# Kernel tuning notes

Hardware: AMD Instinct MI355X
Metric: run time of the kernel (lower is better)

Reference implementation:

```python
import jax, jax.numpy as jnp
import numpy as np
from functools import partial

IN_CH, OUT_CH, HID = 16, 20, 256
B, T = 64, 4096
LEAKY_SLOPE = 0.01  # torch LeakyReLU default


def _lstm_layer(x_seq, Wih, Whh, bih, bhh):
    """Single-layer LSTM over a full sequence.

    x_seq: (T, B, Din). Weights use PyTorch layout: W (4H, Din/H), gate order i,f,g,o.
    Returns hidden states (T, B, H).
    """
    H = Whh.shape[1]
    Tlen, Bsz = x_seq.shape[0], x_seq.shape[1]
    # Precompute input contributions for all timesteps in one GEMM.
    xw = jnp.einsum('tbd,gd->tbg', x_seq, Wih) + (bih + bhh)  # (T, B, 4H)

    def step(carry, xw_t):
        h, c = carry
        gates = xw_t + h @ Whh.T  # (B, 4H)
        i, f, g, o = jnp.split(gates, 4, axis=-1)
        i = jax.nn.sigmoid(i)
        f = jax.nn.sigmoid(f)
        g = jnp.tanh(g)
        o = jax.nn.sigmoid(o)
        c = f * c + i * g
        h = o * jnp.tanh(c)
        return (h, c), h

    h0 = jnp.zeros((Bsz, H), dtype=x_seq.dtype)
    c0 = jnp.zeros((Bsz, H), dtype=x_seq.dtype)
    _, hs = jax.lax.scan(step, (h0, c0), xw)
    return hs  # (T, B, H)


def setup_inputs() -> dict:
    key = jax.random.key(0)
    ks = jax.random.split(key, 12)
    s = 1.0 / np.sqrt(HID)  # torch nn.LSTM init scale
    return {
        'x': jax.random.normal(ks[0], (B, IN_CH, T), dtype=jnp.float32),
        'Wih0': jax.random.normal(ks[1], (4 * HID, IN_CH), dtype=jnp.float32) * s,
        'Whh0': jax.random.normal(ks[2], (4 * HID, HID), dtype=jnp.float32) * s,
        'bih0': jax.random.normal(ks[3], (4 * HID,), dtype=jnp.float32) * s,
        'bhh0': jax.random.normal(ks[4], (4 * HID,), dtype=jnp.float32) * s,
        'Wih1': jax.random.normal(ks[5], (4 * HID, HID), dtype=jnp.float32) * s,
        'Whh1': jax.random.normal(ks[6], (4 * HID, HID), dtype=jnp.float32) * s,
        'bih1': jax.random.normal(ks[7], (4 * HID,), dtype=jnp.float32) * s,
        'bhh1': jax.random.normal(ks[8], (4 * HID,), dtype=jnp.float32) * s,
        'Whead': jax.random.normal(ks[9], (OUT_CH, HID), dtype=jnp.float32) * s,
        'bhead': jax.random.normal(ks[10], (OUT_CH,), dtype=jnp.float32) * s,
    }


def reference(x, Wih0, Whh0, bih0, bhh0, Wih1, Whh1, bih1, bhh1, Whead, bhead):
    # x: (B, C_in, T) -> time-major (T, B, C_in)
    xs = jnp.transpose(x, (2, 0, 1))
    h1 = _lstm_layer(xs, Wih0, Whh0, bih0, bhh0)   # (T, B, H)
    h2 = _lstm_layer(h1, Wih1, Whh1, bih1, bhh1)   # (T, B, H)
    # Head: LeakyReLU then Linear, applied per timestep (vectorized).
    a = jnp.where(h2 >= 0, h2, LEAKY_SLOPE * h2)
    y = jnp.einsum('tbh,oh->tbo', a, Whead) + bhead  # (T, B, OUT)
    return jnp.transpose(y, (1, 2, 0))  # (B, C_out, T)
```

## Files before the change

### kernel.cpp

```cpp
#include <hip/hip_runtime.h>
#include <hip/hip_fp16.h>
#include <stdint.h>


#define T_SEQ 4096
#define NB    64
#define HID   256
#define G4    1024
#define INCH  16
#define OC    20

typedef _Float16 h2v   __attribute__((ext_vector_type(2)));
typedef _Float16 f16x8 __attribute__((ext_vector_type(8)));
typedef float    f32x4 __attribute__((ext_vector_type(4)));

__device__ __forceinline__ float fdot2(uint32_t a, uint32_t b, float c) {
  return __builtin_amdgcn_fdot2(__builtin_bit_cast(h2v, a),
                                __builtin_bit_cast(h2v, b), c, false);
}
__device__ __forceinline__ float sigf(float x) {
  x = fminf(fmaxf(x, -30.f), 30.f);
  return 1.f / (1.f + __expf(-x));
}
__device__ __forceinline__ float tanhf_fast(float x) {
  x = fminf(fmaxf(x, -15.f), 15.f);
  float e = __expf(-2.f * x);
  return (1.f - e) / (1.f + e);
}

#define PIN(x) asm volatile("" : "+v"(x))

struct SmemR {
  __half w[256 * 264];
  uint32_t hbuf[2][144];
  float bsum[1024];
  union {
    uint32_t xb[512 * 8];
    struct {
      __half abuf[2][320];
      __half whd[20 * 264];
      float  bh[20];
    } h1;
  } u;
};
struct SmemG {
  __half a[128 * 40];
  __half b[64 * 40];
};
union Smem { SmemR r; SmemG g; };

struct Params {
  const float* x;
  const __half *wh0, *wh1, *wi0, *wi1, *whd;
  const float  *bs0, *bs1, *bhd;
  float *h0s, *c0s, *h1s, *c1s;
  __half* h1w; const __half* h1r;
  float* xww;  const float* xwr;
  float* y;
  int L, Tc, nch;
};

template <int LAYER>
__device__ void role_rec(SmemR& S, int ch, const Params& P, int b) {
  if (ch < 0 || ch >= P.nch) return;
  const int tid   = threadIdx.x;
  const int slice = tid & 3;
  const int rg    = tid >> 2;
  const int Tc    = P.Tc;
  const __half* whh = (LAYER == 0) ? P.wh0 : P.wh1;

  for (int i = tid; i < 8192; i += 512) {
    int R = i >> 5, oct = i & 31;
    *(uint4*)&S.w[R * 264 + oct * 8] =
        *((const uint4*)(whh + (768 + R) * 256) + oct);
  }
  {
    const float* bs = (LAYER == 0) ? P.bs0 : P.bs1;
    for (int i = tid; i < 1024; i += 512) S.bsum[i] = bs[i];
  }
  const int t0 = ch * Tc;
  if (LAYER == 0) {
    for (int i = tid; i < Tc * 8; i += 512) {
      int dp = i / Tc, tt = i - dp * Tc;
      float v0 = P.x[(b * INCH + 2 * dp) * T_SEQ + t0 + tt];
      float v1 = P.x[(b * INCH + 2 * dp + 1) * T_SEQ + t0 + tt];
      uint32_t pv = (uint32_t)__half_as_ushort(__float2half(v0)) |
                    ((uint32_t)__half_as_ushort(__float2half(v1)) << 16);
      S.u.xb[tt * 8 + dp] = pv;
    }
  } else {
    for (int i = tid; i < OC * 256; i += 512) {
      int o = i >> 8, k = i & 255;
      S.u.h1.whd[o * 264 + k] = P.whd[i];
    }
    if (tid < OC) S.u.h1.bh[tid] = P.bhd[tid];
  }

  uint32_t wr[6][32];
#pragma unroll
  for (int j = 0; j < 6; j++) {
    const uint4* p = (const uint4*)(whh + (rg + 128 * j) * 256 + slice * 64);
#pragma unroll
    for (int q = 0; q < 8; q++) {
      uint4 v = p[q];
      wr[j][4 * q] = v.x; wr[j][4 * q + 1] = v.y;
      wr[j][4 * q + 2] = v.z; wr[j][4 * q + 3] = v.w;
    }
  }
#pragma unroll
  for (int j = 0; j < 6; j++)
#pragma unroll
    for (int q = 0; q < 32; q++) PIN(wr[j][q]);

  uint32_t wx[8][2];
  if (LAYER == 0) {
#pragma unroll
    for (int j = 0; j < 8; j++) {
      const uint32_t* p = (const uint32_t*)(P.wi0 + (rg + 128 * j) * INCH + slice * 4);
      wx[j][0] = p[0]; wx[j][1] = p[1];
    }
#pragma unroll
    for (int j = 0; j < 8; j++) { PIN(wx[j][0]); PIN(wx[j][1]); }
  }

  float* hs = (LAYER == 0) ? P.h0s : P.h1s;
  float* cs = (LAYER == 0) ? P.c0s : P.c1s;
  float hA = 0.f, hB = 0.f, cA = 0.f, cB = 0.f;
  if (slice == 0) {
    if (ch != 0) {
      hA = hs[b * 256 + rg];       cA = cs[b * 256 + rg];
      hB = hs[b * 256 + rg + 128]; cB = cs[b * 256 + rg + 128];
    }
    __half* hb = (__half*)S.hbuf[0];
    hb[(rg >> 6) * 72 + (rg & 63)] = __float2half(hA);
    hb[(2 + (rg >> 6)) * 72 + (rg & 63)] = __float2half(hB);
  }
  float xwpre[8];
  if (LAYER == 1 && slice == 0) {
#pragma unroll
    for (int j = 0; j < 8; j++)
      xwpre[j] = P.xwr[(0 * NB + b) * G4 + rg + 128 * j];
  }
  __syncthreads();

  for (int tt = 0; tt < Tc; ++tt) {
    const __half* hb = (const __half*)S.hbuf[tt & 1];
    float acc[8];
#pragma unroll
    for (int j = 0; j < 8; j++) acc[j] = 0.f;

#pragma unroll
    for (int hf = 0; hf < 2; ++hf) {
      uint32_t hh[16];
      const uint4* hp = (const uint4*)(hb + slice * 72 + hf * 32);
#pragma unroll
      for (int q = 0; q < 4; q++) {
        uint4 v = hp[q];
        hh[4 * q] = v.x; hh[4 * q + 1] = v.y; hh[4 * q + 2] = v.z; hh[4 * q + 3] = v.w;
      }
#pragma unroll
      for (int j = 0; j < 6; j++) {
        float a = acc[j];
#pragma unroll
        for (int q = 0; q < 16; q++) a = fdot2(wr[j][hf * 16 + q], hh[q], a);
        acc[j] = a;
      }
#pragma unroll
      for (int j = 6; j < 8; j++) {
        const uint4* wp =
            (const uint4*)&S.w[((j - 6) * 128 + rg) * 264 + slice * 64 + hf * 32];
        float a = acc[j];
#pragma unroll
        for (int q = 0; q < 4; q++) {
          uint4 v = wp[q];
          a = fdot2(v.x, hh[4 * q], a);
          a = fdot2(v.y, hh[4 * q + 1], a);
          a = fdot2(v.z, hh[4 * q + 2], a);
          a = fdot2(v.w, hh[4 * q + 3], a);
        }
        acc[j] = a;
      }
    }
    if (LAYER == 0) {
      uint32_t xv0 = S.u.xb[tt * 8 + 2 * slice];
      uint32_t xv1 = S.u.xb[tt * 8 + 2 * slice + 1];
#pragma unroll
      for (int j = 0; j < 8; j++) {
        acc[j] = fdot2(wx[j][0], xv0, acc[j]);
        acc[j] = fdot2(wx[j][1], xv1, acc[j]);
      }
    }
#pragma unroll
    for (int j = 0; j < 8; j++) {
      acc[j] += __shfl_xor(acc[j], 1);
      acc[j] += __shfl_xor(acc[j], 2);
    }

    if (slice == 0) {
      float g[8];
#pragma unroll
      for (int j = 0; j < 8; j++) g[j] = acc[j] + S.bsum[rg + 128 * j];
      if (LAYER == 1) {
#pragma unroll
        for (int j = 0; j < 8; j++) g[j] += xwpre[j];
        if (tt + 1 < Tc) {
#pragma unroll
          for (int j = 0; j < 8; j++)
            xwpre[j] = P.xwr[((tt + 1) * NB + b) * G4 + rg + 128 * j];
        }
      }
      float iA = sigf(g[0]), iB = sigf(g[1]);
      float fA = sigf(g[2]), fB = sigf(g[3]);
      float gA = tanhf_fast(g[4]), gB = tanhf_fast(g[5]);
      float oA = sigf(g[6]), oB = sigf(g[7]);
      cA = fA * cA + iA * gA;
      cB = fB * cB + iB * gB;
      hA = oA * tanhf_fast(cA);
      hB = oB * tanhf_fast(cB);
      __half hA16 = __float2half(hA), hB16 = __float2half(hB);
      __half* hw = (__half*)S.hbuf[(tt + 1) & 1];
      hw[(rg >> 6) * 72 + (rg & 63)] = hA16;
      hw[(2 + (rg >> 6)) * 72 + (rg & 63)] = hB16;
      if (LAYER == 0) {
        __half* dst = P.h1w + (size_t)(tt * NB + b) * 256;
        dst[rg] = hA16;
        dst[rg + 128] = hB16;
      } else {
        float aA = hA > 0.f ? hA : 0.01f * hA;
        float aB = hB > 0.f ? hB : 0.01f * hB;
        __half* ab = S.u.h1.abuf[tt & 1];
        ab[(rg >> 5) * 40 + (rg & 31)] = __float2half(aA);
        ab[(4 + (rg >> 5)) * 40 + (rg & 31)] = __float2half(aB);
      }
    }
    __syncthreads();

    if (LAYER == 1 && tid < OC * 8) {
      int o = tid >> 3, ks = tid & 7;
      const uint4* wp = (const uint4*)&S.u.h1.whd[o * 264 + ks * 32];
      const uint4* ap = (const uint4*)&S.u.h1.abuf[tt & 1][ks * 40];
      float a = 0.f;
#pragma unroll
      for (int q = 0; q < 4; q++) {
        uint4 w4 = wp[q];
        uint4 a4 = ap[q];
        a = fdot2(w4.x, a4.x, a);
        a = fdot2(w4.y, a4.y, a);
        a = fdot2(w4.z, a4.z, a);
        a = fdot2(w4.w, a4.w, a);
      }
      a += __shfl_xor(a, 1);
      a += __shfl_xor(a, 2);
      a += __shfl_xor(a, 4);
      if (ks == 0) P.y[(b * OC + o) * T_SEQ + t0 + tt] = a + S.u.h1.bh[o];
    }
  }
  if (slice == 0) {
    hs[b * 256 + rg] = hA;        cs[b * 256 + rg] = cA;
    hs[b * 256 + rg + 128] = hB;  cs[b * 256 + rg + 128] = cB;
  }
}

__device__ void role_gemm(SmemG& S, int chG, const Params& P) {
  if (chG < 0 || chG >= P.nch) return;
  const int bid = blockIdx.x - 128;
  const int nt = bid & 15, mt = bid >> 4;
  const int tb0 = mt * 128, g0 = nt * 64;
  const int tid = threadIdx.x, lane = tid & 63, w = tid >> 6;
  const int wm = w & 3, wn = w >> 2;

  f32x4 cacc[2][2] = {};
  for (int kk = 0; kk < 256; kk += 32) {
    __syncthreads();
    {
      int row = tid >> 2, q = tid & 3;
      const uint4* src = (const uint4*)(P.h1r + (tb0 + row) * 256 + kk + q * 8);
      *(uint4*)&S.a[row * 40 + q * 8] = *src;
    }
    if (tid < 256) {
      int row = tid >> 2, q = tid & 3;
      const uint4* src = (const uint4*)(P.wi1 + (g0 + row) * 256 + kk + q * 8);
      *(uint4*)&S.b[row * 40 + q * 8] = *src;
    }
    __syncthreads();
    f16x8 af[2], bf[2];
#pragma unroll
    for (int mi = 0; mi < 2; mi++)
      af[mi] = *(const f16x8*)&S.a[(wm * 32 + mi * 16 + (lane & 15)) * 40 + (lane >> 4) * 8];
#pragma unroll
    for (int ni = 0; ni < 2; ni++)
      bf[ni] = *(const f16x8*)&S.b[(wn * 32 + ni * 16 + (lane & 15)) * 40 + (lane >> 4) * 8];
#pragma unroll
    for (int mi = 0; mi < 2; mi++)
#pragma unroll
      for (int ni = 0; ni < 2; ni++)
        cacc[mi][ni] = __builtin_amdgcn_mfma_f32_16x16x32_f16(af[mi], bf[ni], cacc[mi][ni], 0, 0, 0);
  }
#pragma unroll
  for (int mi = 0; mi < 2; mi++)
#pragma unroll
    for (int ni = 0; ni < 2; ni++) {
      int m = wm * 32 + mi * 16 + (lane >> 4) * 4;
      int n = g0 + wn * 32 + ni * 16 + (lane & 15);
#pragma unroll
      for (int r = 0; r < 4; r++)
        P.xww[(size_t)(tb0 + m + r) * G4 + n] = cacc[mi][ni][r];
    }
}

__global__ __launch_bounds__(512)
__attribute__((amdgpu_waves_per_eu(2, 2)))
void fused_kernel(Params P) {
  __shared__ Smem S;
  int bid = blockIdx.x;
  if (bid < 64)        role_rec<0>(S.r, P.L, P, bid);
  else if (bid < 128)  role_rec<1>(S.r, P.L - 2, P, bid - 64);
  else                 role_gemm(S.g, P.L - 1, P);
}

__global__ void prep_kernel(const float* Wih0, const float* Whh0,
                            const float* bih0, const float* bhh0,
                            const float* Wih1, const float* Whh1,
                            const float* bih1, const float* bhh1,
                            const float* Whead, const float* bhead,
                            __half* wh0, __half* wh1, __half* wi1, __half* wi0,
                            __half* whd, float* bs0, float* bs1, float* bhd) {
  int i = blockIdx.x * blockDim.x + threadIdx.x;
  if (i < G4 * HID) {
    wh0[i] = __float2half(Whh0[i]);
    wh1[i] = __float2half(Whh1[i]);
    wi1[i] = __float2half(Wih1[i]);
  }
  if (i < G4 * INCH) wi0[i] = __float2half(Wih0[i]);
  if (i < OC * HID)  whd[i] = __float2half(Whead[i]);
  if (i < G4) { bs0[i] = bih0[i] + bhh0[i]; bs1[i] = bih1[i] + bhh1[i]; }
  if (i < OC) bhd[i] = bhead[i];
}

extern "C" void kernel_launch(void* const* d_in, const int* in_sizes, int n_in,
                              void* d_out, int out_size, void* d_ws, size_t ws_size,
                              hipStream_t stream) {
  const float* x     = (const float*)d_in[0];
  const float* Wih0  = (const float*)d_in[1];
  const float* Whh0  = (const float*)d_in[2];
  const float* bih0  = (const float*)d_in[3];
  const float* bhh0  = (const float*)d_in[4];
  const float* Wih1  = (const float*)d_in[5];
  const float* Whh1  = (const float*)d_in[6];
  const float* bih1  = (const float*)d_in[7];
  const float* bhh1  = (const float*)d_in[8];
  const float* Whead = (const float*)d_in[9];
  const float* bhead = (const float*)d_in[10];
  float* y = (float*)d_out;

  char* ws = (char*)d_ws;
  size_t cur = 0;
  auto alloc = [&](size_t sz) -> char* {
    char* p = ws + cur;
    cur = (cur + sz + 255) & ~(size_t)255;
    return p;
  };
  __half* wh0 = (__half*)alloc(G4 * HID * 2);
  __half* wh1 = (__half*)alloc(G4 * HID * 2);
  __half* wi1 = (__half*)alloc(G4 * HID * 2);
  __half* wi0 = (__half*)alloc(G4 * INCH * 2);
  __half* whd = (__half*)alloc(OC * HID * 2);
  float* bs0 = (float*)alloc(G4 * 4);
  float* bs1 = (float*)alloc(G4 * 4);
  float* bhd = (float*)alloc(OC * 4);
  float* h0s = (float*)alloc(NB * HID * 4);
  float* c0s = (float*)alloc(NB * HID * 4);
  float* h1s = (float*)alloc(NB * HID * 4);
  float* c1s = (float*)alloc(NB * HID * 4);
  size_t fixed = cur;

  int Tc = 512;
  while (Tc > 64) {
    size_t need = fixed + 2 * ((size_t)Tc * NB * HID * 2 + 512) +
                  2 * ((size_t)Tc * NB * G4 * 4 + 512);
    if (need <= ws_size) break;
    Tc >>= 1;
  }
  __half* h1buf[2];
  float* xwbuf[2];
  h1buf[0] = (__half*)alloc((size_t)Tc * NB * HID * 2);
  h1buf[1] = (__half*)alloc((size_t)Tc * NB * HID * 2);
  xwbuf[0] = (float*)alloc((size_t)Tc * NB * G4 * 4);
  xwbuf[1] = (float*)alloc((size_t)Tc * NB * G4 * 4);

  const int nch = T_SEQ / Tc;

  prep_kernel<<<(G4 * HID + 255) / 256, 256, 0, stream>>>(
      Wih0, Whh0, bih0, bhh0, Wih1, Whh1, bih1, bhh1, Whead, bhead,
      wh0, wh1, wi1, wi0, whd, bs0, bs1, bhd);

  const int ngemm = Tc * 8;
  for (int L = 0; L < nch + 2; ++L) {
    Params P;
    P.x = x;
    P.wh0 = wh0; P.wh1 = wh1; P.wi0 = wi0; P.wi1 = wi1; P.whd = whd;
    P.bs0 = bs0; P.bs1 = bs1; P.bhd = bhd;
    P.h0s = h0s; P.c0s = c0s; P.h1s = h1s; P.c1s = c1s;
    P.h1w = h1buf[L & 1];
    P.h1r = h1buf[(L + 1) & 1];
    P.xww = xwbuf[(L + 1) & 1];
    P.xwr = xwbuf[L & 1];
    P.y = y;
    P.L = L; P.Tc = Tc; P.nch = nch;
    fused_kernel<<<128 + ngemm, 512, 0, stream>>>(P);
  }
}
```

Measured before the change: 10.87 ms.

## Store xw in fp16, distribute bias/xw adds across slices, swizzle LDS weights

The precomputed input-projection buffer for layer 1 is stored in fp16 instead of fp32, halving its global traffic and workspace, which may also allow a larger time chunk. Bias and xw terms are now added per slice before the shuffle reduction, so all four lanes share the loads instead of slice 0 doing eight serial global loads. The shared-memory copy of the last two gate blocks is re-laid out so each lane reads contiguous 16-byte words, and the hidden-state and activation buffer strides are padded to change bank mapping. The cost is reduced precision of the xw term.

```diff
diff --git a/kernel.cpp b/kernel.cpp
--- a/kernel.cpp
+++ b/kernel.cpp
@@ -31,13 +31,12 @@
 #define PIN(x) asm volatile("" : "+v"(x))
 
 struct SmemR {
-  __half w[256 * 264];
-  uint32_t hbuf[2][144];
-  float bsum[1024];
+  uint32_t w[8 * 16 * 256];
+  __half hbuf[2][4 * 80];
   union {
     uint32_t xb[512 * 8];
     struct {
-      __half abuf[2][320];
+      __half abuf[2][8 * 48];
       __half whd[20 * 264];
       float  bh[20];
     } h1;
@@ -55,7 +54,7 @@
   const float  *bs0, *bs1, *bhd;
   float *h0s, *c0s, *h1s, *c1s;
   __half* h1w; const __half* h1r;
-  float* xww;  const float* xwr;
+  __half* xww; const __half* xwr;
   float* y;
   int L, Tc, nch;
 };
@@ -66,18 +65,22 @@
   const int tid   = threadIdx.x;
   const int slice = tid & 3;
   const int rg    = tid >> 2;
+  const int wv    = tid >> 6;
+  const int ln    = tid & 63;
   const int Tc    = P.Tc;
   const __half* whh = (LAYER == 0) ? P.wh0 : P.wh1;
 
-  for (int i = tid; i < 8192; i += 512) {
-    int R = i >> 5, oct = i & 31;
-    *(uint4*)&S.w[R * 264 + oct * 8] =
-        *((const uint4*)(whh + (768 + R) * 256) + oct);
-  }
-  {
-    const float* bs = (LAYER == 0) ? P.bs0 : P.bs1;
-    for (int i = tid; i < 1024; i += 512) S.bsum[i] = bs[i];
-  }
+#pragma unroll
+  for (int j = 0; j < 2; j++)
+#pragma unroll
+    for (int hf = 0; hf < 2; hf++)
+#pragma unroll
+      for (int q = 0; q < 4; q++) {
+        const uint4 v = *(const uint4*)(whh + (768 + j * 128 + rg) * 256 +
+                                        slice * 64 + hf * 32 + q * 8);
+        *(uint4*)&S.w[(wv * 16 + j * 8 + hf * 4 + q) * 256 + ln * 4] = v;
+      }
+
   const int t0 = ch * Tc;
   if (LAYER == 0) {
     for (int i = tid; i < Tc * 8; i += 512) {
@@ -96,6 +99,13 @@
     if (tid < OC) S.u.h1.bh[tid] = P.bhd[tid];
   }
 
+  float bA, bB;
+  {
+    const float* bs = (LAYER == 0) ? P.bs0 : P.bs1;
+    bA = bs[rg + 256 * slice];
+    bB = bs[rg + 128 + 256 * slice];
+  }
+
   uint32_t wr[6][32];
 #pragma unroll
   for (int j = 0; j < 6; j++) {
@@ -131,20 +141,20 @@
       hA = hs[b * 256 + rg];       cA = cs[b * 256 + rg];
       hB = hs[b * 256 + rg + 128]; cB = cs[b * 256 + rg + 128];
     }
-    __half* hb = (__half*)S.hbuf[0];
-    hb[(rg >> 6) * 72 + (rg & 63)] = __float2half(hA);
-    hb[(2 + (rg >> 6)) * 72 + (rg & 63)] = __float2half(hB);
-  }
-  float xwpre[8];
-  if (LAYER == 1 && slice == 0) {
-#pragma unroll
-    for (int j = 0; j < 8; j++)
-      xwpre[j] = P.xwr[(0 * NB + b) * G4 + rg + 128 * j];
+    __half* hb = S.hbuf[0];
+    hb[(rg >> 6) * 80 + (rg & 63)] = __float2half(hA);
+    hb[(2 + (rg >> 6)) * 80 + (rg & 63)] = __float2half(hB);
+  }
+  float xwA = 0.f, xwB = 0.f;
+  if (LAYER == 1) {
+    const __half* base = P.xwr + (size_t)b * G4;
+    xwA = __half2float(base[rg + 256 * slice]);
+    xwB = __half2float(base[rg + 128 + 256 * slice]);
   }
   __syncthreads();
 
   for (int tt = 0; tt < Tc; ++tt) {
-    const __half* hb = (const __half*)S.hbuf[tt & 1];
+    const __half* hb = S.hbuf[tt & 1];
     float acc[8];
 #pragma unroll
     for (int j = 0; j < 8; j++) acc[j] = 0.f;
@@ -152,7 +162,7 @@
 #pragma unroll
     for (int hf = 0; hf < 2; ++hf) {
       uint32_t hh[16];
-      const uint4* hp = (const uint4*)(hb + slice * 72 + hf * 32);
+      const uint4* hp = (const uint4*)(hb + slice * 80 + hf * 32);
 #pragma unroll
       for (int q = 0; q < 4; q++) {
         uint4 v = hp[q];
@@ -166,19 +176,17 @@
         acc[j] = a;
       }
 #pragma unroll
-      for (int j = 6; j < 8; j++) {
-        const uint4* wp =
-            (const uint4*)&S.w[((j - 6) * 128 + rg) * 264 + slice * 64 + hf * 32];
-        float a = acc[j];
+      for (int j = 0; j < 2; j++) {
+        float a = acc[6 + j];
 #pragma unroll
         for (int q = 0; q < 4; q++) {
-          uint4 v = wp[q];
+          const uint4 v = *(const uint4*)&S.w[(wv * 16 + j * 8 + hf * 4 + q) * 256 + ln * 4];
           a = fdot2(v.x, hh[4 * q], a);
           a = fdot2(v.y, hh[4 * q + 1], a);
           a = fdot2(v.z, hh[4 * q + 2], a);
           a = fdot2(v.w, hh[4 * q + 3], a);
         }
-        acc[j] = a;
+        acc[6 + j] = a;
       }
     }
     if (LAYER == 0) {
@@ -190,6 +198,17 @@
         acc[j] = fdot2(wx[j][1], xv1, acc[j]);
       }
     }
+    acc[2 * slice] += bA;
+    acc[2 * slice + 1] += bB;
+    if (LAYER == 1) {
+      acc[2 * slice] += xwA;
+      acc[2 * slice + 1] += xwB;
+      if (tt + 1 < Tc) {
+        const __half* base = P.xwr + ((size_t)(tt + 1) * NB + b) * G4;
+        xwA = __half2float(base[rg + 256 * slice]);
+        xwB = __half2float(base[rg + 128 + 256 * slice]);
+      }
+    }
 #pragma unroll
     for (int j = 0; j < 8; j++) {
       acc[j] += __shfl_xor(acc[j], 1);
@@ -197,30 +216,18 @@
     }
 
     if (slice == 0) {
-      float g[8];
-#pragma unroll
-      for (int j = 0; j < 8; j++) g[j] = acc[j] + S.bsum[rg + 128 * j];
-      if (LAYER == 1) {
-#pragma unroll
-        for (int j = 0; j < 8; j++) g[j] += xwpre[j];
-        if (tt + 1 < Tc) {
-#pragma unroll
-          for (int j = 0; j < 8; j++)
-            xwpre[j] = P.xwr[((tt + 1) * NB + b) * G4 + rg + 128 * j];
-        }
-      }
-      float iA = sigf(g[0]), iB = sigf(g[1]);
-      float fA = sigf(g[2]), fB = sigf(g[3]);
-      float gA = tanhf_fast(g[4]), gB = tanhf_fast(g[5]);
-      float oA = sigf(g[6]), oB = sigf(g[7]);
+      float iA = sigf(acc[0]), iB = sigf(acc[1]);
+      float fA = sigf(acc[2]), fB = sigf(acc[3]);
+      float gA = tanhf_fast(acc[4]), gB = tanhf_fast(acc[5]);
+      float oA = sigf(acc[6]), oB = sigf(acc[7]);
       cA = fA * cA + iA * gA;
       cB = fB * cB + iB * gB;
       hA = oA * tanhf_fast(cA);
       hB = oB * tanhf_fast(cB);
       __half hA16 = __float2half(hA), hB16 = __float2half(hB);
-      __half* hw = (__half*)S.hbuf[(tt + 1) & 1];
-      hw[(rg >> 6) * 72 + (rg & 63)] = hA16;
-      hw[(2 + (rg >> 6)) * 72 + (rg & 63)] = hB16;
+      __half* hw = S.hbuf[(tt + 1) & 1];
+      hw[(rg >> 6) * 80 + (rg & 63)] = hA16;
+      hw[(2 + (rg >> 6)) * 80 + (rg & 63)] = hB16;
       if (LAYER == 0) {
         __half* dst = P.h1w + (size_t)(tt * NB + b) * 256;
         dst[rg] = hA16;
@@ -229,8 +236,8 @@
         float aA = hA > 0.f ? hA : 0.01f * hA;
         float aB = hB > 0.f ? hB : 0.01f * hB;
         __half* ab = S.u.h1.abuf[tt & 1];
-        ab[(rg >> 5) * 40 + (rg & 31)] = __float2half(aA);
-        ab[(4 + (rg >> 5)) * 40 + (rg & 31)] = __float2half(aB);
+        ab[(rg >> 5) * 48 + (rg & 31)] = __float2half(aA);
+        ab[(4 + (rg >> 5)) * 48 + (rg & 31)] = __float2half(aB);
       }
     }
     __syncthreads();
@@ -238,7 +245,7 @@
     if (LAYER == 1 && tid < OC * 8) {
       int o = tid >> 3, ks = tid & 7;
       const uint4* wp = (const uint4*)&S.u.h1.whd[o * 264 + ks * 32];
-      const uint4* ap = (const uint4*)&S.u.h1.abuf[tt & 1][ks * 40];
+      const uint4* ap = (const uint4*)&S.u.h1.abuf[tt & 1][ks * 48];
       float a = 0.f;
 #pragma unroll
       for (int q = 0; q < 4; q++) {
@@ -304,7 +311,7 @@
       int n = g0 + wn * 32 + ni * 16 + (lane & 15);
 #pragma unroll
       for (int r = 0; r < 4; r++)
-        P.xww[(size_t)(tb0 + m + r) * G4 + n] = cacc[mi][ni][r];
+        P.xww[(size_t)(tb0 + m + r) * G4 + n] = __float2half(cacc[mi][ni][r]);
     }
 }
 
@@ -377,16 +384,16 @@
   int Tc = 512;
   while (Tc > 64) {
     size_t need = fixed + 2 * ((size_t)Tc * NB * HID * 2 + 512) +
-                  2 * ((size_t)Tc * NB * G4 * 4 + 512);
+                  2 * ((size_t)Tc * NB * G4 * 2 + 512);
     if (need <= ws_size) break;
     Tc >>= 1;
   }
   __half* h1buf[2];
-  float* xwbuf[2];
+  __half* xwbuf[2];
   h1buf[0] = (__half*)alloc((size_t)Tc * NB * HID * 2);
   h1buf[1] = (__half*)alloc((size_t)Tc * NB * HID * 2);
-  xwbuf[0] = (float*)alloc((size_t)Tc * NB * G4 * 4);
-  xwbuf[1] = (float*)alloc((size_t)Tc * NB * G4 * 4);
+  xwbuf[0] = (__half*)alloc((size_t)Tc * NB * G4 * 2);
+  xwbuf[1] = (__half*)alloc((size_t)Tc * NB * G4 * 2);
 
   const int nch = T_SEQ / Tc;
 
```

New measurement: 27.23 ms. +150.5%, slower.
